# Kernel tuning notes

Measured on AMD Instinct MI355X. Metric: run time of the kernel, lower is better.

The kernel has to match this reference:

```python
import jax, jax.numpy as jnp
import numpy as np

N = 50000          # nodes
E = 800000         # edges
D_IN, D_HID, D_OUT = 256, 128, 64
NUM_GRAPHS = 16
BN_EPS = 1e-5


def gcn_conv(x, src, dst, W, b, n_nodes):
    """PyG GCNConv: add self-loops, sym-normalized aggregation, then bias."""
    loop = jnp.arange(n_nodes, dtype=src.dtype)
    s = jnp.concatenate([src, loop])
    d = jnp.concatenate([dst, loop])
    deg = jax.ops.segment_sum(jnp.ones_like(s, dtype=x.dtype), d, num_segments=n_nodes)
    dinv = jax.lax.rsqrt(jnp.maximum(deg, 1.0))  # deg >= 1 due to self-loops
    norm = dinv[s] * dinv[d]                      # [E+N]
    h = x @ W                                     # [N, out]
    msg = h[s] * norm[:, None]                    # gather + scale
    out = jax.ops.segment_sum(msg, d, num_segments=n_nodes)
    return out + b


def batch_norm(x, gamma, beta):
    mu = jnp.mean(x, axis=0)
    var = jnp.mean(jnp.square(x - mu), axis=0)
    return (x - mu) * jax.lax.rsqrt(var + BN_EPS) * gamma + beta


def setup_inputs() -> dict:
    key = jax.random.key(0)
    ks = jax.random.split(key, 10)
    x = jax.random.normal(ks[0], (N, D_IN), dtype=jnp.float32)
    edge_index = jax.random.randint(ks[1], (2, E), 0, N, dtype=jnp.int64)
    batch = jnp.sort(jax.random.randint(ks[2], (N,), 0, NUM_GRAPHS, dtype=jnp.int64))
    def glorot(k, fan_in, fan_out):
        lim = np.sqrt(6.0 / (fan_in + fan_out))
        return jax.random.uniform(k, (fan_in, fan_out), jnp.float32, -lim, lim)
    return {
        "x": x, "edge_index": edge_index, "batch": batch,
        "W1": glorot(ks[3], D_IN, D_HID),  "b1": jnp.zeros((D_HID,), jnp.float32),
        "W2": glorot(ks[4], D_HID, D_HID), "b2": jnp.zeros((D_HID,), jnp.float32),
        "W3": glorot(ks[5], D_HID, D_OUT), "b3": jnp.zeros((D_OUT,), jnp.float32),
        "g1": jnp.ones((D_HID,), jnp.float32), "be1": jnp.zeros((D_HID,), jnp.float32),
        "g2": jnp.ones((D_HID,), jnp.float32), "be2": jnp.zeros((D_HID,), jnp.float32),
    }


def reference(x, edge_index, batch, W1, b1, W2, b2, W3, b3, g1, be1, g2, be2):
    src, dst = edge_index[0], edge_index[1]
    n = x.shape[0]
    h = gcn_conv(x, src, dst, W1, b1, n)
    h = jax.nn.relu(batch_norm(h, g1, be1))
    h = gcn_conv(h, src, dst, W2, b2, n)
    h = jax.nn.relu(batch_norm(h, g2, be2))
    h = gcn_conv(h, src, dst, W3, b3, n)          # [N, D_OUT]
    # global mean pool over graph ids
    sums = jax.ops.segment_sum(h, batch, num_segments=NUM_GRAPHS)
    cnts = jax.ops.segment_sum(jnp.ones((n,), h.dtype), batch, num_segments=NUM_GRAPHS)
    return sums / jnp.maximum(cnts, 1.0)[:, None]  # [NUM_GRAPHS, D_OUT]
```

## Files before the change

kernel.cpp:

```cpp
#include <hip/hip_runtime.h>
#include <hip/hip_bf16.h>

#define D_IN   256
#define D_HID  128
#define D_OUT_ 64
#define NGRAPH 16
#define BN_EPS 1e-5f

typedef __attribute__((ext_vector_type(8))) short short8;
typedef __attribute__((ext_vector_type(4))) float floatx4;

__device__ __forceinline__ unsigned short f2bf(float x) {
    unsigned u = __float_as_uint(x);
    return (unsigned short)((u + 0x7fffu + ((u >> 16) & 1u)) >> 16);
}
__device__ __forceinline__ unsigned pack2bf(float lo, float hi) {
    return (unsigned)f2bf(lo) | ((unsigned)f2bf(hi) << 16);
}
__device__ __forceinline__ void bf2_decode(unsigned u, float& lo, float& hi) {
    lo = __uint_as_float(u << 16);
    hi = __uint_as_float(u & 0xffff0000u);
}
__device__ __forceinline__ void accum8(float* acc, uint4 qv, float wt) {
    float f0,f1,f2,f3,f4,f5,f6,f7;
    bf2_decode(qv.x, f0, f1); bf2_decode(qv.y, f2, f3);
    bf2_decode(qv.z, f4, f5); bf2_decode(qv.w, f6, f7);
    acc[0]=fmaf(f0,wt,acc[0]); acc[1]=fmaf(f1,wt,acc[1]);
    acc[2]=fmaf(f2,wt,acc[2]); acc[3]=fmaf(f3,wt,acc[3]);
    acc[4]=fmaf(f4,wt,acc[4]); acc[5]=fmaf(f5,wt,acc[5]);
    acc[6]=fmaf(f6,wt,acc[6]); acc[7]=fmaf(f7,wt,acc[7]);
}

__global__ void prep_kernel(const float* __restrict__ W1, const float* __restrict__ W2,
                            const float* __restrict__ W3,
                            unsigned short* __restrict__ Wt1,
                            unsigned short* __restrict__ Wt2,
                            unsigned short* __restrict__ Wt3,
                            const int* __restrict__ dst, int E, int WB,
                            int* __restrict__ deg, int* __restrict__ rank) {
    const int S1 = D_IN * D_HID, S2 = D_HID * D_HID, S3 = D_HID * D_OUT_;
    if ((int)blockIdx.x < WB) {
        int idx = blockIdx.x * 256 + threadIdx.x;
        if (idx < S1) {
            int k = idx / D_HID, n = idx - k * D_HID;
            Wt1[(size_t)n * D_IN + k] = f2bf(W1[idx]);
        } else if (idx < S1 + S2) {
            int i = idx - S1; int k = i / D_HID, n = i - k * D_HID;
            Wt2[(size_t)n * D_HID + k] = f2bf(W2[i]);
        } else if (idx < S1 + S2 + S3) {
            int i = idx - S1 - S2; int k = i / D_OUT_, n = i - k * D_OUT_;
            Wt3[(size_t)n * D_HID + k] = f2bf(W3[i]);
        }
    } else {
        int e = ((int)blockIdx.x - WB) * 256 + threadIdx.x;
        if (e < E) rank[e] = atomicAdd(&deg[dst[e]], 1);
    }
}

__global__ void dinv_bsum_kernel(const int* __restrict__ deg, int N,
                                 float* __restrict__ dinvp, int* __restrict__ bsum) {
    __shared__ int red[256];
    int t = threadIdx.x;
    int base = blockIdx.x * 1024 + t;
    int s = 0;
    #pragma unroll
    for (int i = 0; i < 4; ++i) {
        int idx = base + i * 256;
        if (idx < N) {
            int d = deg[idx];
            dinvp[idx] = rsqrtf((float)(d + 1));
            s += d;
        }
    }
    red[t] = s;
    __syncthreads();
    for (int off = 128; off > 0; off >>= 1) {
        if (t < off) red[t] += red[t + off];
        __syncthreads();
    }
    if (t == 0) bsum[blockIdx.x] = red[0];
}

__global__ void scan_bsum_kernel(const int* __restrict__ bsum, int NB,
                                 int* __restrict__ bprefix,
                                 int* __restrict__ rowstart, int N, int E) {
    __shared__ int part[256];
    int t = threadIdx.x;
    int s = (t < NB) ? bsum[t] : 0;
    part[t] = s;
    __syncthreads();
    for (int off = 1; off < 256; off <<= 1) {
        int x = (t >= off) ? part[t - off] : 0;
        __syncthreads();
        part[t] += x;
        __syncthreads();
    }
    if (t < NB) bprefix[t] = part[t] - s;
    if (t == 0) rowstart[N] = E;
}

__global__ void local_scan_kernel(const int* __restrict__ deg, int N,
                                  const int* __restrict__ bprefix,
                                  int* __restrict__ rowstart) {
    __shared__ int part[256];
    int t = threadIdx.x;
    int base = blockIdx.x * 1024 + t * 4;
    int v[4]; int s = 0;
    #pragma unroll
    for (int i = 0; i < 4; ++i) {
        v[i] = (base + i < N) ? deg[base + i] : 0;
        s += v[i];
    }
    part[t] = s;
    __syncthreads();
    for (int off = 1; off < 256; off <<= 1) {
        int x = (t >= off) ? part[t - off] : 0;
        __syncthreads();
        part[t] += x;
        __syncthreads();
    }
    int excl = part[t] - s + bprefix[blockIdx.x];
    #pragma unroll
    for (int i = 0; i < 4; ++i) {
        if (base + i < N) rowstart[base + i] = excl;
        excl += v[i];
    }
}

template<int K, int NOUT, int FUSE, int ABF16>
__device__ __forceinline__ void gemm_body(
        int bid, const void* __restrict__ Aptr, const unsigned short* __restrict__ Wt,
        unsigned short* __restrict__ Cb, int M,
        const float* __restrict__ sums, const float* __restrict__ sumsq,
        const float* __restrict__ gam, const float* __restrict__ bet, float invN,
        float* s_sc, float* s_sh) {
    constexpr int NT = NOUT / 16;
    constexpr int KS = K / 32;
    if (FUSE) {
        int t = threadIdx.x;
        if (t < K) {
            float mu  = sums[t] * invN;
            float var = sumsq[t] * invN - mu * mu;
            float sc  = gam[t] * rsqrtf(var + BN_EPS);
            s_sc[t] = sc;
            s_sh[t] = fmaf(-mu, sc, bet[t]);
        }
        __syncthreads();
    }
    int lane = threadIdx.x & 63;
    int wave = threadIdx.x >> 6;
    int col  = lane & 15;
    int quad = lane >> 4;
    int kq   = quad * 8;
    int row  = bid * 64 + wave * 16 + col;
    int rowc = min(row, M - 1);

    short8 afr[KS];
    if (ABF16) {
        const unsigned short* Ab = (const unsigned short*)Aptr;
        uint4 q[KS];
        #pragma unroll
        for (int i = 0; i < KS; ++i)
            q[i] = *(const uint4*)&Ab[(size_t)rowc * K + i * 32 + kq];
        __builtin_amdgcn_sched_barrier(0);
        #pragma unroll
        for (int i = 0; i < KS; ++i) {
            if (FUSE) {
                int kb = i * 32 + kq;
                float f0,f1,f2,f3,f4,f5,f6,f7;
                bf2_decode(q[i].x, f0, f1); bf2_decode(q[i].y, f2, f3);
                bf2_decode(q[i].z, f4, f5); bf2_decode(q[i].w, f6, f7);
                float4 sc0 = *(const float4*)&s_sc[kb];
                float4 sc1 = *(const float4*)&s_sc[kb + 4];
                float4 sh0 = *(const float4*)&s_sh[kb];
                float4 sh1 = *(const float4*)&s_sh[kb + 4];
                f0 = fmaxf(0.f, fmaf(f0, sc0.x, sh0.x));
                f1 = fmaxf(0.f, fmaf(f1, sc0.y, sh0.y));
                f2 = fmaxf(0.f, fmaf(f2, sc0.z, sh0.z));
                f3 = fmaxf(0.f, fmaf(f3, sc0.w, sh0.w));
                f4 = fmaxf(0.f, fmaf(f4, sc1.x, sh1.x));
                f5 = fmaxf(0.f, fmaf(f5, sc1.y, sh1.y));
                f6 = fmaxf(0.f, fmaf(f6, sc1.z, sh1.z));
                f7 = fmaxf(0.f, fmaf(f7, sc1.w, sh1.w));
                uint4 p;
                p.x = pack2bf(f0, f1); p.y = pack2bf(f2, f3);
                p.z = pack2bf(f4, f5); p.w = pack2bf(f6, f7);
                afr[i] = __builtin_bit_cast(short8, p);
            } else {
                afr[i] = __builtin_bit_cast(short8, q[i]);
            }
        }
    } else {
        const float* Af = (const float*)Aptr;
        float4 a0[KS], a1[KS];
        #pragma unroll
        for (int i = 0; i < KS; ++i) {
            a0[i] = *(const float4*)&Af[(size_t)rowc * K + i * 32 + kq];
            a1[i] = *(const float4*)&Af[(size_t)rowc * K + i * 32 + kq + 4];
        }
        __builtin_amdgcn_sched_barrier(0);
        #pragma unroll
        for (int i = 0; i < KS; ++i) {
            uint4 p;
            p.x = pack2bf(a0[i].x, a0[i].y); p.y = pack2bf(a0[i].z, a0[i].w);
            p.z = pack2bf(a1[i].x, a1[i].y); p.w = pack2bf(a1[i].z, a1[i].w);
            afr[i] = __builtin_bit_cast(short8, p);
        }
    }

    floatx4 acc[NT];
    #pragma unroll
    for (int nt = 0; nt < NT; ++nt) acc[nt] = (floatx4){0.f, 0.f, 0.f, 0.f};

    #pragma unroll
    for (int i = 0; i < KS; ++i) {
        #pragma unroll
        for (int nt = 0; nt < NT; ++nt) {
            short8 bfrag = *(const short8*)&Wt[(size_t)(nt * 16 + col) * K + i * 32 + kq];
            acc[nt] = __builtin_amdgcn_mfma_f32_16x16x32_bf16(afr[i], bfrag, acc[nt], 0, 0, 0);
        }
    }

    int obase = bid * 64 + wave * 16 + quad * 4;
    #pragma unroll
    for (int r = 0; r < 4; ++r) {
        int orow = obase + r;
        if (orow < M) {
            #pragma unroll
            for (int nt = 0; nt < NT; ++nt)
                Cb[(size_t)orow * NOUT + nt * 16 + col] = f2bf(acc[nt][r]);
        }
    }
}

template<int K, int NOUT, int FUSE, int ABF16>
__global__ __launch_bounds__(256, 3) void gemm_mfma_kernel(
        const void* __restrict__ Aptr, const unsigned short* __restrict__ Wt,
        unsigned short* __restrict__ Cb, int M,
        const float* __restrict__ sums, const float* __restrict__ sumsq,
        const float* __restrict__ gam, const float* __restrict__ bet, float invN) {
    __shared__ float s_sc[FUSE ? K : 1];
    __shared__ float s_sh[FUSE ? K : 1];
    gemm_body<K, NOUT, FUSE, ABF16>(blockIdx.x, Aptr, Wt, Cb, M,
                                    sums, sumsq, gam, bet, invN, s_sc, s_sh);
}

__global__ __launch_bounds__(256, 3) void gemm1_scatter_kernel(
        const float* __restrict__ x, const unsigned short* __restrict__ Wt1,
        unsigned short* __restrict__ Cb, int M, int GB,
        const int* __restrict__ src, const int* __restrict__ dst, int E,
        const int* __restrict__ rowstart, const int* __restrict__ rank,
        int* __restrict__ csr) {
    if ((int)blockIdx.x < GB) {
        gemm_body<D_IN, D_HID, 0, 0>(blockIdx.x, x, Wt1, Cb, M,
                                     nullptr, nullptr, nullptr, nullptr, 0.f,
                                     nullptr, nullptr);
    } else {
        int e = ((int)blockIdx.x - GB) * 256 + threadIdx.x;
        if (e < E) {
            int d = dst[e];
            csr[rowstart[d] + rank[e]] = src[e];
        }
    }
}

template<int D>
__global__ __launch_bounds__(256) void agg_bf16_kernel(
        const unsigned short* __restrict__ h, const float* __restrict__ dinvp,
        const int* __restrict__ rowstart, const int* __restrict__ csr,
        const float* __restrict__ bias,
        unsigned short* __restrict__ outb, int N) {
    constexpr int LPR = D / 8;
    constexpr int RPB = 256 / LPR;
    int lane = threadIdx.x & (LPR - 1);
    int r    = threadIdx.x / LPR;
    int v = blockIdx.x * RPB + r;
    if (v >= N) return;
    int c0 = lane * 8;
    const unsigned short* hc = h + c0;
    float dv = dinvp[v];

    float acc[8];
    {
        float w = dv * dv;
        uint4 q = *(const uint4*)&hc[(size_t)v * D];
        float4 b0 = *(const float4*)&bias[c0];
        float4 b1 = *(const float4*)&bias[c0 + 4];
        acc[0]=b0.x; acc[1]=b0.y; acc[2]=b0.z; acc[3]=b0.w;
        acc[4]=b1.x; acc[5]=b1.y; acc[6]=b1.z; acc[7]=b1.w;
        accum8(acc, q, w);
    }
    int j  = rowstart[v];
    int j1 = rowstart[v + 1];
    for (; j + 8 <= j1; j += 8) {
        int   s[8]; float w[8]; uint4 q[8];
        #pragma unroll
        for (int i = 0; i < 8; ++i) s[i] = csr[j + i];
        #pragma unroll
        for (int i = 0; i < 8; ++i) q[i] = *(const uint4*)&hc[(size_t)s[i] * D];
        #pragma unroll
        for (int i = 0; i < 8; ++i) w[i] = dinvp[s[i]] * dv;
        #pragma unroll
        for (int i = 0; i < 8; ++i) accum8(acc, q[i], w[i]);
    }
    for (; j + 4 <= j1; j += 4) {
        int s0 = csr[j],     s1 = csr[j + 1];
        int s2 = csr[j + 2], s3 = csr[j + 3];
        float w0 = dinvp[s0] * dv, w1 = dinvp[s1] * dv;
        float w2 = dinvp[s2] * dv, w3 = dinvp[s3] * dv;
        uint4 q0 = *(const uint4*)&hc[(size_t)s0 * D];
        uint4 q1 = *(const uint4*)&hc[(size_t)s1 * D];
        uint4 q2 = *(const uint4*)&hc[(size_t)s2 * D];
        uint4 q3 = *(const uint4*)&hc[(size_t)s3 * D];
        accum8(acc, q0, w0); accum8(acc, q1, w1);
        accum8(acc, q2, w2); accum8(acc, q3, w3);
    }
    for (; j < j1; ++j) {
        int s = csr[j];
        float w = dinvp[s] * dv;
        uint4 q = *(const uint4*)&hc[(size_t)s * D];
        accum8(acc, q, w);
    }
    uint4 o;
    o.x = pack2bf(acc[0], acc[1]); o.y = pack2bf(acc[2], acc[3]);
    o.z = pack2bf(acc[4], acc[5]); o.w = pack2bf(acc[6], acc[7]);
    *(uint4*)&outb[(size_t)v * D + c0] = o;
}

__global__ void bn_stats_bf16_kernel(const unsigned short* __restrict__ x, int N,
                                     float* __restrict__ sums, float* __restrict__ sumsq) {
    __shared__ float ls0[256], ls1[256], lq0[256], lq1[256];
    int pr = threadIdx.x & 63;
    int rg = threadIdx.x >> 6;
    float s0=0.f, s1=0.f, q0=0.f, q1=0.f;
    for (int v = blockIdx.x * 4 + rg; v < N; v += gridDim.x * 4) {
        unsigned u = *(const unsigned*)&x[(size_t)v * 128 + pr * 2];
        float lo, hi; bf2_decode(u, lo, hi);
        s0 += lo; s1 += hi;
        q0 = fmaf(lo, lo, q0); q1 = fmaf(hi, hi, q1);
    }
    ls0[threadIdx.x]=s0; ls1[threadIdx.x]=s1; lq0[threadIdx.x]=q0; lq1[threadIdx.x]=q1;
    __syncthreads();
    if (threadIdx.x < 64) {
        int pp = threadIdx.x;
        float a0=0,a1=0,b0=0,b1=0;
        #pragma unroll
        for (int g = 0; g < 4; ++g) {
            a0 += ls0[g*64+pp]; a1 += ls1[g*64+pp];
            b0 += lq0[g*64+pp]; b1 += lq1[g*64+pp];
        }
        atomicAdd(&sums[pp*2],  a0); atomicAdd(&sums[pp*2+1],  a1);
        atomicAdd(&sumsq[pp*2], b0); atomicAdd(&sumsq[pp*2+1], b1);
    }
}

__global__ void pool_bf16_kernel(const unsigned short* __restrict__ x,
                                 const int* __restrict__ batch, int N,
                                 float* __restrict__ psum, int* __restrict__ pcnt,
                                 int* __restrict__ done, float* __restrict__ out) {
    __shared__ float ls[NGRAPH * 64];
    __shared__ int   lc[NGRAPH];
    __shared__ int   is_last;
    for (int i = threadIdx.x; i < NGRAPH * 64; i += blockDim.x) ls[i] = 0.f;
    if (threadIdx.x < NGRAPH) lc[threadIdx.x] = 0;
    __syncthreads();
    int total = N * 32;
    for (int idx = blockIdx.x * blockDim.x + threadIdx.x; idx < total;
         idx += gridDim.x * blockDim.x) {
        int v = idx >> 5, cp = idx & 31;
        unsigned u = *(const unsigned*)&x[(size_t)v * 64 + cp * 2];
        float lo, hi; bf2_decode(u, lo, hi);
        int g = batch[v];
        atomicAdd(&ls[g * 64 + cp * 2],     lo);
        atomicAdd(&ls[g * 64 + cp * 2 + 1], hi);
        if (cp == 0) atomicAdd(&lc[g], 1);
    }
    __syncthreads();
    for (int i = threadIdx.x; i < NGRAPH * 64; i += blockDim.x) atomicAdd(&psum[i], ls[i]);
    if (threadIdx.x < NGRAPH) atomicAdd(&pcnt[threadIdx.x], lc[threadIdx.x]);

    __threadfence();
    if (threadIdx.x == 0)
        is_last = (atomicAdd(done, 1) == (int)gridDim.x - 1) ? 1 : 0;
    __syncthreads();
    if (is_last) {
        __threadfence();
        for (int i = threadIdx.x; i < NGRAPH * 64; i += blockDim.x) {
            int g = i >> 6;
            float s = atomicAdd(&psum[i], 0.f);
            int   c = atomicAdd(&pcnt[g], 0);
            out[i] = s / (float)max(c, 1);
        }
    }
}

extern "C" void kernel_launch(void* const* d_in, const int* in_sizes, int n_in,
                              void* d_out, int out_size, void* d_ws, size_t ws_size,
                              hipStream_t stream) {
    const float* x   = (const float*)d_in[0];
    const int*   ei  = (const int*)d_in[1];
    const int*   bat = (const int*)d_in[2];
    const float* W1  = (const float*)d_in[3];
    const float* b1  = (const float*)d_in[4];
    const float* W2  = (const float*)d_in[5];
    const float* b2  = (const float*)d_in[6];
    const float* W3  = (const float*)d_in[7];
    const float* b3  = (const float*)d_in[8];
    const float* g1  = (const float*)d_in[9];
    const float* be1 = (const float*)d_in[10];
    const float* g2  = (const float*)d_in[11];
    const float* be2 = (const float*)d_in[12];
    float* out = (float*)d_out;

    int N = in_sizes[0] / D_IN;
    int E = in_sizes[1] / 2;
    const int* src = ei;
    const int* dst = ei + E;

    char* p = (char*)d_ws;
    auto alloc = [&](size_t bytes) { char* r = p; p += (bytes + 255) & ~(size_t)255; return r; };
    int NB = (N + 1023) / 1024;
    char* zbase = p;
    int*   deg    = (int*)  alloc((size_t)N * 4);
    float* sums1  = (float*)alloc(128 * 4);
    float* sumsq1 = (float*)alloc(128 * 4);
    float* sums2  = (float*)alloc(128 * 4);
    float* sumsq2 = (float*)alloc(128 * 4);
    float* psum   = (float*)alloc(NGRAPH * 64 * 4);
    int*   pcnt   = (int*)  alloc(NGRAPH * 4);
    int*   done   = (int*)  alloc(256);
    size_t zspan  = (size_t)(p - zbase);
    int*   rowstart = (int*)  alloc((size_t)(N + 1) * 4);
    int*   rank     = (int*)  alloc((size_t)E * 4);
    float* dinvp    = (float*)alloc((size_t)N * 4);
    int*   bsum     = (int*)  alloc((size_t)NB * 4);
    int*   bprefix  = (int*)  alloc((size_t)NB * 4);
    int*   csr      = (int*)  alloc((size_t)E * 4);
    unsigned short* hb16   = (unsigned short*)alloc((size_t)N * 128 * 2);
    unsigned short* aggb16 = (unsigned short*)alloc((size_t)N * 128 * 2);
    unsigned short* Wt1 = (unsigned short*)alloc((size_t)D_HID * D_IN * 2);
    unsigned short* Wt2 = (unsigned short*)alloc((size_t)D_HID * D_HID * 2);
    unsigned short* Wt3 = (unsigned short*)alloc((size_t)D_OUT_ * D_HID * 2);

    int ebl = (E + 255) / 256;
    int gblocks = (N + 63) / 64;
    int wtot = D_IN * D_HID + D_HID * D_HID + D_HID * D_OUT_;
    int wblocks = (wtot + 255) / 256;
    float invN = 1.0f / (float)N;

    (void)hipMemsetAsync(zbase, 0, zspan, stream);

    prep_kernel<<<wblocks + ebl, 256, 0, stream>>>(
        W1, W2, W3, Wt1, Wt2, Wt3, dst, E, wblocks, deg, rank);
    dinv_bsum_kernel<<<NB, 256, 0, stream>>>(deg, N, dinvp, bsum);
    scan_bsum_kernel<<<1, 256, 0, stream>>>(bsum, NB, bprefix, rowstart, N, E);
    local_scan_kernel<<<NB, 256, 0, stream>>>(deg, N, bprefix, rowstart);

    gemm1_scatter_kernel<<<gblocks + ebl, 256, 0, stream>>>(
        x, Wt1, hb16, N, gblocks, src, dst, E, rowstart, rank, csr);

    agg_bf16_kernel<D_HID><<<(N + 15) / 16, 256, 0, stream>>>(
        hb16, dinvp, rowstart, csr, b1, aggb16, N);
    bn_stats_bf16_kernel<<<256, 256, 0, stream>>>(aggb16, N, sums1, sumsq1);

    gemm_mfma_kernel<D_HID, D_HID, 1, 1><<<gblocks, 256, 0, stream>>>(
        aggb16, Wt2, hb16, N, sums1, sumsq1, g1, be1, invN);
    agg_bf16_kernel<D_HID><<<(N + 15) / 16, 256, 0, stream>>>(
        hb16, dinvp, rowstart, csr, b2, aggb16, N);
    bn_stats_bf16_kernel<<<256, 256, 0, stream>>>(aggb16, N, sums2, sumsq2);

    gemm_mfma_kernel<D_HID, D_OUT_, 1, 1><<<gblocks, 256, 0, stream>>>(
        aggb16, Wt3, hb16, N, sums2, sumsq2, g2, be2, invN);
    agg_bf16_kernel<D_OUT_><<<(N + 31) / 32, 256, 0, stream>>>(
        hb16, dinvp, rowstart, csr, b3, aggb16, N);

    pool_bf16_kernel<<<256, 256, 0, stream>>>(aggb16, bat, N, psum, pcnt, done, out);
}
```

Before: 398.4 us.

## Fuse final aggregation with mean pooling and merge scan kernels

```diff
diff --git a/kernel.cpp b/kernel.cpp
--- a/kernel.cpp
+++ b/kernel.cpp
@@ -31,30 +31,10 @@
     acc[6]=fmaf(f6,wt,acc[6]); acc[7]=fmaf(f7,wt,acc[7]);
 }
 
-__global__ void prep_kernel(const float* __restrict__ W1, const float* __restrict__ W2,
-                            const float* __restrict__ W3,
-                            unsigned short* __restrict__ Wt1,
-                            unsigned short* __restrict__ Wt2,
-                            unsigned short* __restrict__ Wt3,
-                            const int* __restrict__ dst, int E, int WB,
-                            int* __restrict__ deg, int* __restrict__ rank) {
-    const int S1 = D_IN * D_HID, S2 = D_HID * D_HID, S3 = D_HID * D_OUT_;
-    if ((int)blockIdx.x < WB) {
-        int idx = blockIdx.x * 256 + threadIdx.x;
-        if (idx < S1) {
-            int k = idx / D_HID, n = idx - k * D_HID;
-            Wt1[(size_t)n * D_IN + k] = f2bf(W1[idx]);
-        } else if (idx < S1 + S2) {
-            int i = idx - S1; int k = i / D_HID, n = i - k * D_HID;
-            Wt2[(size_t)n * D_HID + k] = f2bf(W2[i]);
-        } else if (idx < S1 + S2 + S3) {
-            int i = idx - S1 - S2; int k = i / D_OUT_, n = i - k * D_OUT_;
-            Wt3[(size_t)n * D_HID + k] = f2bf(W3[i]);
-        }
-    } else {
-        int e = ((int)blockIdx.x - WB) * 256 + threadIdx.x;
-        if (e < E) rank[e] = atomicAdd(&deg[dst[e]], 1);
-    }
+__global__ void count_rank_kernel(const int* __restrict__ dst, int E,
+                                  int* __restrict__ deg, int* __restrict__ rank) {
+    int e = blockIdx.x * blockDim.x + threadIdx.x;
+    if (e < E) rank[e] = atomicAdd(&deg[dst[e]], 1);
 }
 
 __global__ void dinv_bsum_kernel(const int* __restrict__ deg, int N,
@@ -81,29 +61,23 @@
     if (t == 0) bsum[blockIdx.x] = red[0];
 }
 
-__global__ void scan_bsum_kernel(const int* __restrict__ bsum, int NB,
-                                 int* __restrict__ bprefix,
-                                 int* __restrict__ rowstart, int N, int E) {
+__global__ void local_scan2_kernel(const int* __restrict__ deg, int N,
+                                   const int* __restrict__ bsum, int NB,
+                                   int* __restrict__ rowstart, int E) {
     __shared__ int part[256];
+    __shared__ int bpref_s;
     int t = threadIdx.x;
-    int s = (t < NB) ? bsum[t] : 0;
-    part[t] = s;
-    __syncthreads();
-    for (int off = 1; off < 256; off <<= 1) {
-        int x = (t >= off) ? part[t - off] : 0;
+    int val = (t < (int)blockIdx.x && t < NB) ? bsum[t] : 0;
+    part[t] = val;
+    __syncthreads();
+    for (int off = 128; off > 0; off >>= 1) {
+        if (t < off) part[t] += part[t + off];
         __syncthreads();
-        part[t] += x;
-        __syncthreads();
-    }
-    if (t < NB) bprefix[t] = part[t] - s;
-    if (t == 0) rowstart[N] = E;
-}
-
-__global__ void local_scan_kernel(const int* __restrict__ deg, int N,
-                                  const int* __restrict__ bprefix,
-                                  int* __restrict__ rowstart) {
-    __shared__ int part[256];
-    int t = threadIdx.x;
+    }
+    if (t == 0) bpref_s = part[0];
+    __syncthreads();
+    int bpref = bpref_s;
+
     int base = blockIdx.x * 1024 + t * 4;
     int v[4]; int s = 0;
     #pragma unroll
@@ -119,11 +93,31 @@
         part[t] += x;
         __syncthreads();
     }
-    int excl = part[t] - s + bprefix[blockIdx.x];
+    int excl = part[t] - s + bpref;
     #pragma unroll
     for (int i = 0; i < 4; ++i) {
         if (base + i < N) rowstart[base + i] = excl;
         excl += v[i];
+    }
+    if (blockIdx.x == 0 && t == 0) rowstart[N] = E;
+}
+
+__global__ void wprep_all_kernel(const float* __restrict__ W1, const float* __restrict__ W2,
+                                 const float* __restrict__ W3,
+                                 unsigned short* __restrict__ Wt1,
+                                 unsigned short* __restrict__ Wt2,
+                                 unsigned short* __restrict__ Wt3) {
+    int idx = blockIdx.x * blockDim.x + threadIdx.x;
+    const int S1 = D_IN * D_HID, S2 = D_HID * D_HID, S3 = D_HID * D_OUT_;
+    if (idx < S1) {
+        int k = idx / D_HID, n = idx - k * D_HID;
+        Wt1[(size_t)n * D_IN + k] = f2bf(W1[idx]);
+    } else if (idx < S1 + S2) {
+        int i = idx - S1; int k = i / D_HID, n = i - k * D_HID;
+        Wt2[(size_t)n * D_HID + k] = f2bf(W2[i]);
+    } else if (idx < S1 + S2 + S3) {
+        int i = idx - S1 - S2; int k = i / D_OUT_, n = i - k * D_OUT_;
+        Wt3[(size_t)n * D_HID + k] = f2bf(W3[i]);
     }
 }
 
@@ -327,6 +321,85 @@
     *(uint4*)&outb[(size_t)v * D + c0] = o;
 }
 
+__global__ __launch_bounds__(256) void agg3_pool_kernel(
+        const unsigned short* __restrict__ h, const float* __restrict__ dinvp,
+        const int* __restrict__ rowstart, const int* __restrict__ csr,
+        const float* __restrict__ bias, const int* __restrict__ batch, int N,
+        float* __restrict__ psum, int* __restrict__ pcnt,
+        int* __restrict__ done, float* __restrict__ out, int nblocks) {
+    __shared__ float ls[NGRAPH * 64];
+    __shared__ int   lc[NGRAPH];
+    __shared__ int   is_last;
+    for (int i = threadIdx.x; i < NGRAPH * 64; i += 256) ls[i] = 0.f;
+    if (threadIdx.x < NGRAPH) lc[threadIdx.x] = 0;
+    __syncthreads();
+
+    constexpr int D = D_OUT_;
+    int lane = threadIdx.x & 7;
+    int r    = threadIdx.x >> 3;
+    int v = blockIdx.x * 32 + r;
+    if (v < N) {
+        int c0 = lane * 8;
+        const unsigned short* hc = h + c0;
+        float dv = dinvp[v];
+        float acc[8];
+        {
+            float w = dv * dv;
+            uint4 q = *(const uint4*)&hc[(size_t)v * D];
+            float4 b0 = *(const float4*)&bias[c0];
+            float4 b1 = *(const float4*)&bias[c0 + 4];
+            acc[0]=b0.x; acc[1]=b0.y; acc[2]=b0.z; acc[3]=b0.w;
+            acc[4]=b1.x; acc[5]=b1.y; acc[6]=b1.z; acc[7]=b1.w;
+            accum8(acc, q, w);
+        }
+        int j  = rowstart[v];
+        int j1 = rowstart[v + 1];
+        for (; j + 8 <= j1; j += 8) {
+            int   s[8]; float w[8]; uint4 q[8];
+            #pragma unroll
+            for (int i = 0; i < 8; ++i) s[i] = csr[j + i];
+            #pragma unroll
+            for (int i = 0; i < 8; ++i) q[i] = *(const uint4*)&hc[(size_t)s[i] * D];
+            #pragma unroll
+            for (int i = 0; i < 8; ++i) w[i] = dinvp[s[i]] * dv;
+            #pragma unroll
+            for (int i = 0; i < 8; ++i) accum8(acc, q[i], w[i]);
+        }
+        for (; j < j1; ++j) {
+            int s = csr[j];
+            float w = dinvp[s] * dv;
+            uint4 q = *(const uint4*)&hc[(size_t)s * D];
+            accum8(acc, q, w);
+        }
+        int g = batch[v];
+        #pragma unroll
+        for (int i = 0; i < 8; ++i) atomicAdd(&ls[g * 64 + c0 + i], acc[i]);
+        if (lane == 0) atomicAdd(&lc[g], 1);
+    }
+    __syncthreads();
+
+    for (int i = threadIdx.x; i < NGRAPH * 64; i += 256) {
+        float s = ls[i];
+        if (s != 0.f) atomicAdd(&psum[i], s);
+    }
+    if (threadIdx.x < NGRAPH && lc[threadIdx.x] != 0)
+        atomicAdd(&pcnt[threadIdx.x], lc[threadIdx.x]);
+
+    __threadfence();
+    if (threadIdx.x == 0)
+        is_last = (atomicAdd(done, 1) == nblocks - 1) ? 1 : 0;
+    __syncthreads();
+    if (is_last) {
+        __threadfence();
+        for (int i = threadIdx.x; i < NGRAPH * 64; i += 256) {
+            int g = i >> 6;
+            float s = atomicAdd(&psum[i], 0.f);
+            int   c = atomicAdd(&pcnt[g], 0);
+            out[i] = s / (float)max(c, 1);
+        }
+    }
+}
+
 __global__ void bn_stats_bf16_kernel(const unsigned short* __restrict__ x, int N,
                                      float* __restrict__ sums, float* __restrict__ sumsq) {
     __shared__ float ls0[256], ls1[256], lq0[256], lq1[256];
@@ -351,46 +424,6 @@
         }
         atomicAdd(&sums[pp*2],  a0); atomicAdd(&sums[pp*2+1],  a1);
         atomicAdd(&sumsq[pp*2], b0); atomicAdd(&sumsq[pp*2+1], b1);
-    }
-}
-
-__global__ void pool_bf16_kernel(const unsigned short* __restrict__ x,
-                                 const int* __restrict__ batch, int N,
-                                 float* __restrict__ psum, int* __restrict__ pcnt,
-                                 int* __restrict__ done, float* __restrict__ out) {
-    __shared__ float ls[NGRAPH * 64];
-    __shared__ int   lc[NGRAPH];
-    __shared__ int   is_last;
-    for (int i = threadIdx.x; i < NGRAPH * 64; i += blockDim.x) ls[i] = 0.f;
-    if (threadIdx.x < NGRAPH) lc[threadIdx.x] = 0;
-    __syncthreads();
-    int total = N * 32;
-    for (int idx = blockIdx.x * blockDim.x + threadIdx.x; idx < total;
-         idx += gridDim.x * blockDim.x) {
-        int v = idx >> 5, cp = idx & 31;
-        unsigned u = *(const unsigned*)&x[(size_t)v * 64 + cp * 2];
-        float lo, hi; bf2_decode(u, lo, hi);
-        int g = batch[v];
-        atomicAdd(&ls[g * 64 + cp * 2],     lo);
-        atomicAdd(&ls[g * 64 + cp * 2 + 1], hi);
-        if (cp == 0) atomicAdd(&lc[g], 1);
-    }
-    __syncthreads();
-    for (int i = threadIdx.x; i < NGRAPH * 64; i += blockDim.x) atomicAdd(&psum[i], ls[i]);
-    if (threadIdx.x < NGRAPH) atomicAdd(&pcnt[threadIdx.x], lc[threadIdx.x]);
-
-    __threadfence();
-    if (threadIdx.x == 0)
-        is_last = (atomicAdd(done, 1) == (int)gridDim.x - 1) ? 1 : 0;
-    __syncthreads();
-    if (is_last) {
-        __threadfence();
-        for (int i = threadIdx.x; i < NGRAPH * 64; i += blockDim.x) {
-            int g = i >> 6;
-            float s = atomicAdd(&psum[i], 0.f);
-            int   c = atomicAdd(&pcnt[g], 0);
-            out[i] = s / (float)max(c, 1);
-        }
     }
 }
 
@@ -434,7 +467,6 @@
     int*   rank     = (int*)  alloc((size_t)E * 4);
     float* dinvp    = (float*)alloc((size_t)N * 4);
     int*   bsum     = (int*)  alloc((size_t)NB * 4);
-    int*   bprefix  = (int*)  alloc((size_t)NB * 4);
     int*   csr      = (int*)  alloc((size_t)E * 4);
     unsigned short* hb16   = (unsigned short*)alloc((size_t)N * 128 * 2);
     unsigned short* aggb16 = (unsigned short*)alloc((size_t)N * 128 * 2);
@@ -445,16 +477,15 @@
     int ebl = (E + 255) / 256;
     int gblocks = (N + 63) / 64;
     int wtot = D_IN * D_HID + D_HID * D_HID + D_HID * D_OUT_;
-    int wblocks = (wtot + 255) / 256;
+    int nb3 = (N + 31) / 32;
     float invN = 1.0f / (float)N;
 
     (void)hipMemsetAsync(zbase, 0, zspan, stream);
 
-    prep_kernel<<<wblocks + ebl, 256, 0, stream>>>(
-        W1, W2, W3, Wt1, Wt2, Wt3, dst, E, wblocks, deg, rank);
+    wprep_all_kernel<<<(wtot + 255) / 256, 256, 0, stream>>>(W1, W2, W3, Wt1, Wt2, Wt3);
+    count_rank_kernel<<<ebl, 256, 0, stream>>>(dst, E, deg, rank);
     dinv_bsum_kernel<<<NB, 256, 0, stream>>>(deg, N, dinvp, bsum);
-    scan_bsum_kernel<<<1, 256, 0, stream>>>(bsum, NB, bprefix, rowstart, N, E);
-    local_scan_kernel<<<NB, 256, 0, stream>>>(deg, N, bprefix, rowstart);
+    local_scan2_kernel<<<NB, 256, 0, stream>>>(deg, N, bsum, NB, rowstart, E);
 
     gemm1_scatter_kernel<<<gblocks + ebl, 256, 0, stream>>>(
         x, Wt1, hb16, N, gblocks, src, dst, E, rowstart, rank, csr);
@@ -471,8 +502,7 @@
 
     gemm_mfma_kernel<D_HID, D_OUT_, 1, 1><<<gblocks, 256, 0, stream>>>(
         aggb16, Wt3, hb16, N, sums2, sumsq2, g2, be2, invN);
-    agg_bf16_kernel<D_OUT_><<<(N + 31) / 32, 256, 0, stream>>>(
-        hb16, dinvp, rowstart, csr, b3, aggb16, N);
-
-    pool_bf16_kernel<<<256, 256, 0, stream>>>(aggb16, bat, N, psum, pcnt, done, out);
-}
+
+    agg3_pool_kernel<<<nb3, 256, 0, stream>>>(
+        hb16, dinvp, rowstart, csr, b3, bat, N, psum, pcnt, done, out, nb3);
+}
```

Measured after the change: 458.8 us. +15.2%, slower.

## Fold block-prefix scan into local scan and split prep and pool kernels

Applied to the files above, without the earlier changes.

```diff
diff --git a/kernel.cpp b/kernel.cpp
--- a/kernel.cpp
+++ b/kernel.cpp
@@ -31,30 +31,10 @@
     acc[6]=fmaf(f6,wt,acc[6]); acc[7]=fmaf(f7,wt,acc[7]);
 }
 
-__global__ void prep_kernel(const float* __restrict__ W1, const float* __restrict__ W2,
-                            const float* __restrict__ W3,
-                            unsigned short* __restrict__ Wt1,
-                            unsigned short* __restrict__ Wt2,
-                            unsigned short* __restrict__ Wt3,
-                            const int* __restrict__ dst, int E, int WB,
-                            int* __restrict__ deg, int* __restrict__ rank) {
-    const int S1 = D_IN * D_HID, S2 = D_HID * D_HID, S3 = D_HID * D_OUT_;
-    if ((int)blockIdx.x < WB) {
-        int idx = blockIdx.x * 256 + threadIdx.x;
-        if (idx < S1) {
-            int k = idx / D_HID, n = idx - k * D_HID;
-            Wt1[(size_t)n * D_IN + k] = f2bf(W1[idx]);
-        } else if (idx < S1 + S2) {
-            int i = idx - S1; int k = i / D_HID, n = i - k * D_HID;
-            Wt2[(size_t)n * D_HID + k] = f2bf(W2[i]);
-        } else if (idx < S1 + S2 + S3) {
-            int i = idx - S1 - S2; int k = i / D_OUT_, n = i - k * D_OUT_;
-            Wt3[(size_t)n * D_HID + k] = f2bf(W3[i]);
-        }
-    } else {
-        int e = ((int)blockIdx.x - WB) * 256 + threadIdx.x;
-        if (e < E) rank[e] = atomicAdd(&deg[dst[e]], 1);
-    }
+__global__ void count_rank_kernel(const int* __restrict__ dst, int E,
+                                  int* __restrict__ deg, int* __restrict__ rank) {
+    int e = blockIdx.x * blockDim.x + threadIdx.x;
+    if (e < E) rank[e] = atomicAdd(&deg[dst[e]], 1);
 }
 
 __global__ void dinv_bsum_kernel(const int* __restrict__ deg, int N,
@@ -81,12 +61,30 @@
     if (t == 0) bsum[blockIdx.x] = red[0];
 }
 
-__global__ void scan_bsum_kernel(const int* __restrict__ bsum, int NB,
-                                 int* __restrict__ bprefix,
-                                 int* __restrict__ rowstart, int N, int E) {
+__global__ void local_scan2_kernel(const int* __restrict__ deg, int N,
+                                   const int* __restrict__ bsum, int NB,
+                                   int* __restrict__ rowstart, int E) {
     __shared__ int part[256];
+    __shared__ int bpref_s;
     int t = threadIdx.x;
-    int s = (t < NB) ? bsum[t] : 0;
+    int val = (t < (int)blockIdx.x && t < NB) ? bsum[t] : 0;
+    part[t] = val;
+    __syncthreads();
+    for (int off = 128; off > 0; off >>= 1) {
+        if (t < off) part[t] += part[t + off];
+        __syncthreads();
+    }
+    if (t == 0) bpref_s = part[0];
+    __syncthreads();
+    int bpref = bpref_s;
+
+    int base = blockIdx.x * 1024 + t * 4;
+    int v[4]; int s = 0;
+    #pragma unroll
+    for (int i = 0; i < 4; ++i) {
+        v[i] = (base + i < N) ? deg[base + i] : 0;
+        s += v[i];
+    }
     part[t] = s;
     __syncthreads();
     for (int off = 1; off < 256; off <<= 1) {
@@ -95,35 +93,31 @@
         part[t] += x;
         __syncthreads();
     }
-    if (t < NB) bprefix[t] = part[t] - s;
-    if (t == 0) rowstart[N] = E;
-}
-
-__global__ void local_scan_kernel(const int* __restrict__ deg, int N,
-                                  const int* __restrict__ bprefix,
-                                  int* __restrict__ rowstart) {
-    __shared__ int part[256];
-    int t = threadIdx.x;
-    int base = blockIdx.x * 1024 + t * 4;
-    int v[4]; int s = 0;
-    #pragma unroll
-    for (int i = 0; i < 4; ++i) {
-        v[i] = (base + i < N) ? deg[base + i] : 0;
-        s += v[i];
-    }
-    part[t] = s;
-    __syncthreads();
-    for (int off = 1; off < 256; off <<= 1) {
-        int x = (t >= off) ? part[t - off] : 0;
-        __syncthreads();
-        part[t] += x;
-        __syncthreads();
-    }
-    int excl = part[t] - s + bprefix[blockIdx.x];
+    int excl = part[t] - s + bpref;
     #pragma unroll
     for (int i = 0; i < 4; ++i) {
         if (base + i < N) rowstart[base + i] = excl;
         excl += v[i];
+    }
+    if (blockIdx.x == 0 && t == 0) rowstart[N] = E;
+}
+
+__global__ void wprep_all_kernel(const float* __restrict__ W1, const float* __restrict__ W2,
+                                 const float* __restrict__ W3,
+                                 unsigned short* __restrict__ Wt1,
+                                 unsigned short* __restrict__ Wt2,
+                                 unsigned short* __restrict__ Wt3) {
+    int idx = blockIdx.x * blockDim.x + threadIdx.x;
+    const int S1 = D_IN * D_HID, S2 = D_HID * D_HID, S3 = D_HID * D_OUT_;
+    if (idx < S1) {
+        int k = idx / D_HID, n = idx - k * D_HID;
+        Wt1[(size_t)n * D_IN + k] = f2bf(W1[idx]);
+    } else if (idx < S1 + S2) {
+        int i = idx - S1; int k = i / D_HID, n = i - k * D_HID;
+        Wt2[(size_t)n * D_HID + k] = f2bf(W2[i]);
+    } else if (idx < S1 + S2 + S3) {
+        int i = idx - S1 - S2; int k = i / D_OUT_, n = i - k * D_OUT_;
+        Wt3[(size_t)n * D_HID + k] = f2bf(W3[i]);
     }
 }
 
@@ -356,11 +350,9 @@
 
 __global__ void pool_bf16_kernel(const unsigned short* __restrict__ x,
                                  const int* __restrict__ batch, int N,
-                                 float* __restrict__ psum, int* __restrict__ pcnt,
-                                 int* __restrict__ done, float* __restrict__ out) {
+                                 float* __restrict__ psum, int* __restrict__ pcnt) {
     __shared__ float ls[NGRAPH * 64];
     __shared__ int   lc[NGRAPH];
-    __shared__ int   is_last;
     for (int i = threadIdx.x; i < NGRAPH * 64; i += blockDim.x) ls[i] = 0.f;
     if (threadIdx.x < NGRAPH) lc[threadIdx.x] = 0;
     __syncthreads();
@@ -378,20 +370,14 @@
     __syncthreads();
     for (int i = threadIdx.x; i < NGRAPH * 64; i += blockDim.x) atomicAdd(&psum[i], ls[i]);
     if (threadIdx.x < NGRAPH) atomicAdd(&pcnt[threadIdx.x], lc[threadIdx.x]);
-
-    __threadfence();
-    if (threadIdx.x == 0)
-        is_last = (atomicAdd(done, 1) == (int)gridDim.x - 1) ? 1 : 0;
-    __syncthreads();
-    if (is_last) {
-        __threadfence();
-        for (int i = threadIdx.x; i < NGRAPH * 64; i += blockDim.x) {
-            int g = i >> 6;
-            float s = atomicAdd(&psum[i], 0.f);
-            int   c = atomicAdd(&pcnt[g], 0);
-            out[i] = s / (float)max(c, 1);
-        }
-    }
+}
+
+__global__ void pool_final_kernel(const float* __restrict__ psum, const int* __restrict__ pcnt,
+                                  float* __restrict__ out) {
+    int i = threadIdx.x;
+    int g = i >> 6;
+    float cnt = (float)max(pcnt[g], 1);
+    out[i] = psum[i] / cnt;
 }
 
 extern "C" void kernel_launch(void* const* d_in, const int* in_sizes, int n_in,
@@ -428,13 +414,11 @@
     float* sumsq2 = (float*)alloc(128 * 4);
     float* psum   = (float*)alloc(NGRAPH * 64 * 4);
     int*   pcnt   = (int*)  alloc(NGRAPH * 4);
-    int*   done   = (int*)  alloc(256);
     size_t zspan  = (size_t)(p - zbase);
     int*   rowstart = (int*)  alloc((size_t)(N + 1) * 4);
     int*   rank     = (int*)  alloc((size_t)E * 4);
     float* dinvp    = (float*)alloc((size_t)N * 4);
     int*   bsum     = (int*)  alloc((size_t)NB * 4);
-    int*   bprefix  = (int*)  alloc((size_t)NB * 4);
     int*   csr      = (int*)  alloc((size_t)E * 4);
     unsigned short* hb16   = (unsigned short*)alloc((size_t)N * 128 * 2);
     unsigned short* aggb16 = (unsigned short*)alloc((size_t)N * 128 * 2);
@@ -445,16 +429,14 @@
     int ebl = (E + 255) / 256;
     int gblocks = (N + 63) / 64;
     int wtot = D_IN * D_HID + D_HID * D_HID + D_HID * D_OUT_;
-    int wblocks = (wtot + 255) / 256;
     float invN = 1.0f / (float)N;
 
     (void)hipMemsetAsync(zbase, 0, zspan, stream);
 
-    prep_kernel<<<wblocks + ebl, 256, 0, stream>>>(
-        W1, W2, W3, Wt1, Wt2, Wt3, dst, E, wblocks, deg, rank);
+    wprep_all_kernel<<<(wtot + 255) / 256, 256, 0, stream>>>(W1, W2, W3, Wt1, Wt2, Wt3);
+    count_rank_kernel<<<ebl, 256, 0, stream>>>(dst, E, deg, rank);
     dinv_bsum_kernel<<<NB, 256, 0, stream>>>(deg, N, dinvp, bsum);
-    scan_bsum_kernel<<<1, 256, 0, stream>>>(bsum, NB, bprefix, rowstart, N, E);
-    local_scan_kernel<<<NB, 256, 0, stream>>>(deg, N, bprefix, rowstart);
+    local_scan2_kernel<<<NB, 256, 0, stream>>>(deg, N, bsum, NB, rowstart, E);
 
     gemm1_scatter_kernel<<<gblocks + ebl, 256, 0, stream>>>(
         x, Wt1, hb16, N, gblocks, src, dst, E, rowstart, rank, csr);
@@ -474,5 +456,6 @@
     agg_bf16_kernel<D_OUT_><<<(N + 31) / 32, 256, 0, stream>>>(
         hb16, dinvp, rowstart, csr, b3, aggb16, N);
 
-    pool_bf16_kernel<<<256, 256, 0, stream>>>(aggb16, bat, N, psum, pcnt, done, out);
-}
+    pool_bf16_kernel<<<256, 256, 0, stream>>>(aggb16, bat, N, psum, pcnt);
+    pool_final_kernel<<<1, NGRAPH * 64, 0, stream>>>(psum, pcnt, out);
+}
```

After: 386.9 us. -2.9%, faster.
